# Kernel tuning notes

Measured on AMD Instinct MI355X. Metric: run time of the kernel, lower is better.

Reference implementation:

```python
import jax, jax.numpy as jnp
import numpy as np

N_NODES = 100000
N_EDGES = 1600000
NFEAT, NHID, NCLASS = 64, 128, 32


def _glorot(key, shape):
    fan_in, fan_out = shape[0], shape[1]
    lim = np.sqrt(6.0 / (fan_in + fan_out))
    return jax.random.uniform(key, shape, jnp.float32, -lim, lim)


def setup_inputs() -> dict:
    key = jax.random.key(0)
    ks = jax.random.split(key, 12)
    x = jax.random.normal(ks[0], (N_NODES, NFEAT), jnp.float32)
    edge_idx = jax.random.randint(ks[1], (2, N_EDGES), 0, N_NODES, jnp.int64)
    edge_weight = jax.random.uniform(ks[2], (N_EDGES,), jnp.float32)
    return {
        "x": x,
        "edge_idx": edge_idx,
        "edge_weight": edge_weight,
        # SAGEConv 1: out = mean_agg(x) @ Wl1 + b1 + x @ Wr1
        "Wl1": _glorot(ks[3], (NFEAT, NHID)),
        "Wr1": _glorot(ks[4], (NFEAT, NHID)),
        "b1": jnp.zeros((NHID,), jnp.float32),
        # SAGEConv 2
        "Wl2": _glorot(ks[5], (NHID, NHID)),
        "Wr2": _glorot(ks[6], (NHID, NHID)),
        "b2": jnp.zeros((NHID,), jnp.float32),
        # fc head: Linear(nhid, nclass) -> Linear(nclass, 1)
        "Wfc1": _glorot(ks[7], (NHID, NCLASS)),
        "bfc1": jnp.zeros((NCLASS,), jnp.float32),
        "Wfc2": _glorot(ks[8], (NCLASS, 1)),
        "bfc2": jnp.zeros((1,), jnp.float32),
    }


def _sage_conv(x, src, dst, Wl, Wr, b, n_nodes):
    # mean aggregation of source features at destination nodes
    msg_sum = jax.ops.segment_sum(x[src], dst, num_segments=n_nodes)  # [N, d]
    deg = jax.ops.segment_sum(jnp.ones((src.shape[0], 1), x.dtype), dst,
                              num_segments=n_nodes)                    # [N, 1]
    mean = msg_sum / jnp.maximum(deg, 1.0)
    return mean @ Wl + b + x @ Wr


def reference(x, edge_idx, edge_weight, Wl1, Wr1, b1, Wl2, Wr2, b2,
              Wfc1, bfc1, Wfc2, bfc2):
    n_nodes = x.shape[0]
    src, dst = edge_idx[0], edge_idx[1]
    # dropout is identity in eval mode (training=False)
    h = _sage_conv(x, src, dst, Wl1, Wr1, b1, n_nodes)   # [N, nhid]
    h = _sage_conv(h, src, dst, Wl2, Wr2, b2, n_nodes)   # [N, nhid]
    h = h @ Wfc1 + bfc1                                   # [N, nclass]
    out = h @ Wfc2 + bfc2                                 # [N, 1]
    return out
```

## Files before the change

kernel.cpp:

```cpp
#include <hip/hip_runtime.h>

#define S_NODES 512
#define S_SHIFT 9
#define CAP     10240
#define CHUNK   8192
#define NREP    4

__global__ __launch_bounds__(512) void fold_dots_kernel(
    const float* __restrict__ x,
    const float* __restrict__ Wl1, const float* __restrict__ Wr1, const float* __restrict__ b1,
    const float* __restrict__ Wl2, const float* __restrict__ Wr2, const float* __restrict__ b2,
    const float* __restrict__ Wfc1, const float* __restrict__ bfc1,
    const float* __restrict__ Wfc2, const float* __restrict__ bfc2,
    float* __restrict__ ga, float2* __restrict__ gbc, float* __restrict__ c01,
    int* __restrict__ cursor, int N)
{
    __shared__ float u[128], vl2[128], vr2[128], w2[32], wv[192];
    int t = threadIdx.x;
    if (blockIdx.x == 0 && t < 256) cursor[t] = 0;
    if (t < 32) w2[t] = Wfc2[t];
    __syncthreads();
    if (t < 128) {
        float s = 0.f;
        for (int k = 0; k < 32; ++k) s += Wfc1[t * 32 + k] * w2[k];
        u[t] = s;
    }
    __syncthreads();
    if (t < 128) {
        float a = 0.f, b = 0.f;
        for (int k = 0; k < 128; ++k) {
            a += Wl2[t * 128 + k] * u[k];
            b += Wr2[t * 128 + k] * u[k];
        }
        vl2[t] = a; vr2[t] = b;
    }
    __syncthreads();
    if (t < 64) {
        float wa = 0.f, wb = 0.f, wc = 0.f;
        for (int j = 0; j < 128; ++j) {
            float l1 = Wl1[t * 128 + j], r1 = Wr1[t * 128 + j];
            wc += l1 * vl2[j];
            wb += l1 * vr2[j] + r1 * vl2[j];
            wa += r1 * vr2[j];
        }
        wv[t] = wa; wv[64 + t] = wb; wv[128 + t] = wc;
    }
    if (blockIdx.x == 0 && t == 0) {
        float c0 = bfc2[0], c1 = 0.f;
        for (int j = 0; j < 128; ++j) {
            c0 += b1[j] * vr2[j] + b2[j] * u[j];
            c1 += b1[j] * vl2[j];
        }
        for (int k = 0; k < 32; ++k) c0 += bfc1[k] * w2[k];
        c01[0] = c0; c01[1] = c1;
    }
    __syncthreads();
    int lane = t & 63, sub = t >> 6;
    float wa = wv[lane], wb = wv[64 + lane], wc = wv[128 + lane];
    int ngroups = (N + 7) / 8;
    for (int g = blockIdx.x; g < ngroups; g += gridDim.x) {
        int node = g * 8 + sub;
        if (node >= N) continue;
        float v = x[(size_t)node * 64 + lane];
        float a = v * wa, b = v * wb, c = v * wc;
        for (int off = 32; off > 0; off >>= 1) {
            a += __shfl_down(a, off);
            b += __shfl_down(b, off);
            c += __shfl_down(c, off);
        }
        if (lane == 0) { ga[node] = a; gbc[node] = make_float2(b, c); }
    }
}

__global__ __launch_bounds__(256) void scatter_kernel(
    const int* __restrict__ src, const int* __restrict__ dst, int E, int B,
    int* __restrict__ cursor, unsigned* __restrict__ bucket)
{
    __shared__ int hist[256], lbase[256], lcur[256];
    int t = threadIdx.x;
    int e0 = blockIdx.x * CHUNK;
    int cnt = E - e0; if (cnt > CHUNK) cnt = CHUNK;
    hist[t] = 0;
    __syncthreads();
    for (int i = t; i < cnt; i += 256)
        atomicAdd(&hist[dst[e0 + i] >> S_SHIFT], 1);
    __syncthreads();
    if (t < B && hist[t] > 0) lbase[t] = atomicAdd(&cursor[t], hist[t]);
    lcur[t] = 0;
    __syncthreads();
    for (int i = t; i < cnt; i += 256) {
        int d = dst[e0 + i], s = src[e0 + i];
        int b = d >> S_SHIFT;
        int off = atomicAdd(&lcur[b], 1);
        bucket[(size_t)b * CAP + (unsigned)(lbase[b] + off)] =
            ((unsigned)s << S_SHIFT) | (unsigned)(d & (S_NODES - 1));
    }
}

__global__ __launch_bounds__(1024) void aggA_kernel(
    const unsigned* __restrict__ bucket, const int* __restrict__ cursor,
    const float2* __restrict__ gbc, const float* __restrict__ ga,
    const float* __restrict__ c01,
    float* __restrict__ q, float* __restrict__ t1, float* __restrict__ inv, int N)
{
    __shared__ float aB[NREP][S_NODES], aC[NREP][S_NODES];
    __shared__ int cnt[NREP][S_NODES];
    int t = threadIdx.x, b = blockIdx.x;
    int r = (t >> 6) & (NREP - 1);
    for (int i = t; i < NREP * S_NODES; i += 1024) {
        aB[0][i] = 0.f; aC[0][i] = 0.f; cnt[0][i] = 0;
    }
    __syncthreads();
    int n = cursor[b];
    const unsigned* bp = bucket + (size_t)b * CAP;
    for (int i = t; i < n; i += 1024) {
        unsigned uu = bp[i];
        float2 g = gbc[uu >> S_SHIFT];
        int dl = uu & (S_NODES - 1);
        atomicAdd(&aB[r][dl], g.x);
        atomicAdd(&aC[r][dl], g.y);
        atomicAdd(&cnt[r][dl], 1);
    }
    __syncthreads();
    if (t < S_NODES) {
        int node = (b << S_SHIFT) + t;
        if (node < N) {
            float sb = aB[0][t] + aB[1][t] + aB[2][t] + aB[3][t];
            float sc = aC[0][t] + aC[1][t] + aC[2][t] + aC[3][t];
            int d = cnt[0][t] + cnt[1][t] + cnt[2][t] + cnt[3][t];
            float iv = 1.0f / ((d > 0) ? (float)d : 1.0f);
            inv[node] = iv;
            q[node]   = iv * sc;
            t1[node]  = ga[node] + iv * sb + c01[0] + (d > 0 ? c01[1] : 0.f);
        }
    }
}

__global__ __launch_bounds__(1024) void aggB_kernel(
    const unsigned* __restrict__ bucket, const int* __restrict__ cursor,
    const float* __restrict__ q, const float* __restrict__ t1,
    const float* __restrict__ inv, float* __restrict__ out, int N)
{
    __shared__ float a2[NREP][S_NODES];
    int t = threadIdx.x, b = blockIdx.x;
    int r = (t >> 6) & (NREP - 1);
    for (int i = t; i < NREP * S_NODES; i += 1024) a2[0][i] = 0.f;
    __syncthreads();
    int n = cursor[b];
    const unsigned* bp = bucket + (size_t)b * CAP;
    for (int i = t; i < n; i += 1024) {
        unsigned uu = bp[i];
        atomicAdd(&a2[r][uu & (S_NODES - 1)], q[uu >> S_SHIFT]);
    }
    __syncthreads();
    if (t < S_NODES) {
        int node = (b << S_SHIFT) + t;
        if (node < N)
            out[node] = t1[node] + inv[node] * (a2[0][t] + a2[1][t] + a2[2][t] + a2[3][t]);
    }
}

extern "C" void kernel_launch(void* const* d_in, const int* in_sizes, int n_in,
                              void* d_out, int out_size, void* d_ws, size_t ws_size,
                              hipStream_t stream) {
    const float* x    = (const float*)d_in[0];
    const int*   eidx = (const int*)d_in[1];
    const float* Wl1  = (const float*)d_in[3];
    const float* Wr1  = (const float*)d_in[4];
    const float* b1   = (const float*)d_in[5];
    const float* Wl2  = (const float*)d_in[6];
    const float* Wr2  = (const float*)d_in[7];
    const float* b2   = (const float*)d_in[8];
    const float* Wfc1 = (const float*)d_in[9];
    const float* bfc1 = (const float*)d_in[10];
    const float* Wfc2 = (const float*)d_in[11];
    const float* bfc2 = (const float*)d_in[12];

    const int N = in_sizes[0] / 64;
    const int E = in_sizes[2];
    const int* src = eidx;
    const int* dst = eidx + E;
    const int B = (N + S_NODES - 1) / S_NODES;
    const int nscat = (E + CHUNK - 1) / CHUNK;

    char* ws = (char*)d_ws;
    int*      cursor = (int*)(ws);
    float*    c01    = (float*)(ws + 1024);
    float*    ga     = (float*)(ws + 2048);
    float*    q      = (float*)(ws + 2048 + (size_t)N * 4);
    float*    t1     = (float*)(ws + 2048 + (size_t)N * 8);
    float*    inv    = (float*)(ws + 2048 + (size_t)N * 12);
    float2*   gbc    = (float2*)(ws + 2048 + (size_t)N * 16);
    unsigned* bucket = (unsigned*)(ws + 2048 + (size_t)N * 24);

    fold_dots_kernel<<<256, 512, 0, stream>>>(
        x, Wl1, Wr1, b1, Wl2, Wr2, b2, Wfc1, bfc1, Wfc2, bfc2,
        ga, gbc, c01, cursor, N);

    scatter_kernel<<<nscat, 256, 0, stream>>>(src, dst, E, B, cursor, bucket);

    aggA_kernel<<<B, 1024, 0, stream>>>(bucket, cursor, gbc, ga, c01, q, t1, inv, N);
    aggB_kernel<<<B, 1024, 0, stream>>>(bucket, cursor, q, t1, inv, (float*)d_out, N);
}
```

Before: 201.2 us.

## Fuse all stages into one cooperative kernel with grid-wide syncs

Merges the weight folding, per-node dot products, edge bucketing and both aggregation passes into a single cooperative kernel separated by grid.sync, instead of four launches. t1 and inv now stay in shared memory between the two aggregation phases rather than going through global memory. The weight folding is rewritten with wave-level shuffle reductions, and the x dot products use float4 loads. The cursor reset moves to a hipMemsetAsync. In exchange, the grid is capped at 256 blocks of 1024 threads, so the scatter phase loses parallelism, and grid-wide barriers add their own cost.

```diff
diff --git a/kernel.cpp b/kernel.cpp
--- a/kernel.cpp
+++ b/kernel.cpp
@@ -1,162 +1,179 @@
 #include <hip/hip_runtime.h>
-
+#include <hip/hip_cooperative_groups.h>
+
+namespace cg = cooperative_groups;
+
+#define S_SHIFT 9
 #define S_NODES 512
-#define S_SHIFT 9
 #define CAP     10240
-#define CHUNK   8192
+#define CHUNK   2048
 #define NREP    4
-
-__global__ __launch_bounds__(512) void fold_dots_kernel(
+#define GRID    256
+#define BLK     1024
+
+__global__ __launch_bounds__(BLK, 4) void mega_kernel(
     const float* __restrict__ x,
+    const int* __restrict__ src, const int* __restrict__ dst,
+    int E, int N, int B, int nchunk,
+    int* __restrict__ cursor, unsigned* __restrict__ bucket,
     const float* __restrict__ Wl1, const float* __restrict__ Wr1, const float* __restrict__ b1,
     const float* __restrict__ Wl2, const float* __restrict__ Wr2, const float* __restrict__ b2,
     const float* __restrict__ Wfc1, const float* __restrict__ bfc1,
     const float* __restrict__ Wfc2, const float* __restrict__ bfc2,
-    float* __restrict__ ga, float2* __restrict__ gbc, float* __restrict__ c01,
-    int* __restrict__ cursor, int N)
+    float* __restrict__ ga, float2* __restrict__ gbc, float* __restrict__ q,
+    float* __restrict__ out)
 {
-    __shared__ float u[128], vl2[128], vr2[128], w2[32], wv[192];
+    __shared__ float wv[192], c01s[2];
+    __shared__ float uu[128], vl2[128], vr2[128], w2[32];
+    __shared__ int hist[256], lbase[256], lcur[256];
+    __shared__ float aB[NREP][S_NODES], aC[NREP][S_NODES];
+    __shared__ int cnts[NREP][S_NODES];
+    __shared__ float t1s[S_NODES], invs[S_NODES];
+
+    cg::grid_group grid = cg::this_grid();
     int t = threadIdx.x;
-    if (blockIdx.x == 0 && t < 256) cursor[t] = 0;
+    int l = t & 63;
+    int w = t >> 6;
+
     if (t < 32) w2[t] = Wfc2[t];
     __syncthreads();
-    if (t < 128) {
-        float s = 0.f;
-        for (int k = 0; k < 32; ++k) s += Wfc1[t * 32 + k] * w2[k];
-        u[t] = s;
-    }
-    __syncthreads();
-    if (t < 128) {
-        float a = 0.f, b = 0.f;
-        for (int k = 0; k < 128; ++k) {
-            a += Wl2[t * 128 + k] * u[k];
-            b += Wr2[t * 128 + k] * u[k];
-        }
-        vl2[t] = a; vr2[t] = b;
-    }
-    __syncthreads();
-    if (t < 64) {
-        float wa = 0.f, wb = 0.f, wc = 0.f;
-        for (int j = 0; j < 128; ++j) {
-            float l1 = Wl1[t * 128 + j], r1 = Wr1[t * 128 + j];
-            wc += l1 * vl2[j];
-            wb += l1 * vr2[j] + r1 * vl2[j];
-            wa += r1 * vr2[j];
-        }
-        wv[t] = wa; wv[64 + t] = wb; wv[128 + t] = wc;
-    }
-    if (blockIdx.x == 0 && t == 0) {
-        float c0 = bfc2[0], c1 = 0.f;
-        for (int j = 0; j < 128; ++j) {
-            c0 += b1[j] * vr2[j] + b2[j] * u[j];
-            c1 += b1[j] * vl2[j];
-        }
-        for (int k = 0; k < 32; ++k) c0 += bfc1[k] * w2[k];
-        c01[0] = c0; c01[1] = c1;
-    }
-    __syncthreads();
-    int lane = t & 63, sub = t >> 6;
-    float wa = wv[lane], wb = wv[64 + lane], wc = wv[128 + lane];
-    int ngroups = (N + 7) / 8;
-    for (int g = blockIdx.x; g < ngroups; g += gridDim.x) {
-        int node = g * 8 + sub;
-        if (node >= N) continue;
-        float v = x[(size_t)node * 64 + lane];
-        float a = v * wa, b = v * wb, c = v * wc;
-        for (int off = 32; off > 0; off >>= 1) {
-            a += __shfl_down(a, off);
-            b += __shfl_down(b, off);
-            c += __shfl_down(c, off);
-        }
-        if (lane == 0) { ga[node] = a; gbc[node] = make_float2(b, c); }
-    }
-}
-
-__global__ __launch_bounds__(256) void scatter_kernel(
-    const int* __restrict__ src, const int* __restrict__ dst, int E, int B,
-    int* __restrict__ cursor, unsigned* __restrict__ bucket)
-{
-    __shared__ int hist[256], lbase[256], lcur[256];
-    int t = threadIdx.x;
-    int e0 = blockIdx.x * CHUNK;
-    int cnt = E - e0; if (cnt > CHUNK) cnt = CHUNK;
-    hist[t] = 0;
-    __syncthreads();
-    for (int i = t; i < cnt; i += 256)
-        atomicAdd(&hist[dst[e0 + i] >> S_SHIFT], 1);
-    __syncthreads();
-    if (t < B && hist[t] > 0) lbase[t] = atomicAdd(&cursor[t], hist[t]);
-    lcur[t] = 0;
-    __syncthreads();
-    for (int i = t; i < cnt; i += 256) {
-        int d = dst[e0 + i], s = src[e0 + i];
-        int b = d >> S_SHIFT;
-        int off = atomicAdd(&lcur[b], 1);
-        bucket[(size_t)b * CAP + (unsigned)(lbase[b] + off)] =
-            ((unsigned)s << S_SHIFT) | (unsigned)(d & (S_NODES - 1));
-    }
-}
-
-__global__ __launch_bounds__(1024) void aggA_kernel(
-    const unsigned* __restrict__ bucket, const int* __restrict__ cursor,
-    const float2* __restrict__ gbc, const float* __restrict__ ga,
-    const float* __restrict__ c01,
-    float* __restrict__ q, float* __restrict__ t1, float* __restrict__ inv, int N)
-{
-    __shared__ float aB[NREP][S_NODES], aC[NREP][S_NODES];
-    __shared__ int cnt[NREP][S_NODES];
-    int t = threadIdx.x, b = blockIdx.x;
-    int r = (t >> 6) & (NREP - 1);
-    for (int i = t; i < NREP * S_NODES; i += 1024) {
-        aB[0][i] = 0.f; aC[0][i] = 0.f; cnt[0][i] = 0;
-    }
-    __syncthreads();
-    int n = cursor[b];
-    const unsigned* bp = bucket + (size_t)b * CAP;
-    for (int i = t; i < n; i += 1024) {
-        unsigned uu = bp[i];
-        float2 g = gbc[uu >> S_SHIFT];
-        int dl = uu & (S_NODES - 1);
-        atomicAdd(&aB[r][dl], g.x);
-        atomicAdd(&aC[r][dl], g.y);
-        atomicAdd(&cnt[r][dl], 1);
-    }
-    __syncthreads();
-    if (t < S_NODES) {
-        int node = (b << S_SHIFT) + t;
-        if (node < N) {
-            float sb = aB[0][t] + aB[1][t] + aB[2][t] + aB[3][t];
-            float sc = aC[0][t] + aC[1][t] + aC[2][t] + aC[3][t];
-            int d = cnt[0][t] + cnt[1][t] + cnt[2][t] + cnt[3][t];
-            float iv = 1.0f / ((d > 0) ? (float)d : 1.0f);
-            inv[node] = iv;
-            q[node]   = iv * sc;
-            t1[node]  = ga[node] + iv * sb + c01[0] + (d > 0 ? c01[1] : 0.f);
-        }
-    }
-}
-
-__global__ __launch_bounds__(1024) void aggB_kernel(
-    const unsigned* __restrict__ bucket, const int* __restrict__ cursor,
-    const float* __restrict__ q, const float* __restrict__ t1,
-    const float* __restrict__ inv, float* __restrict__ out, int N)
-{
-    __shared__ float a2[NREP][S_NODES];
-    int t = threadIdx.x, b = blockIdx.x;
-    int r = (t >> 6) & (NREP - 1);
-    for (int i = t; i < NREP * S_NODES; i += 1024) a2[0][i] = 0.f;
-    __syncthreads();
-    int n = cursor[b];
-    const unsigned* bp = bucket + (size_t)b * CAP;
-    for (int i = t; i < n; i += 1024) {
-        unsigned uu = bp[i];
-        atomicAdd(&a2[r][uu & (S_NODES - 1)], q[uu >> S_SHIFT]);
-    }
-    __syncthreads();
-    if (t < S_NODES) {
-        int node = (b << S_SHIFT) + t;
-        if (node < N)
-            out[node] = t1[node] + inv[node] * (a2[0][t] + a2[1][t] + a2[2][t] + a2[3][t]);
+    for (int j = 0; j < 8; ++j) {
+        int i = w + 16 * j;
+        float p = (l < 32) ? Wfc1[i * 32 + l] * w2[l] : 0.f;
+        for (int m = 16; m; m >>= 1) p += __shfl_xor(p, m);
+        if (l == 0) uu[i] = p;
+    }
+    __syncthreads();
+    for (int j = 0; j < 8; ++j) {
+        int i = w + 16 * j;
+        float ua = uu[l], ub = uu[64 + l];
+        float pa = Wl2[i * 128 + l] * ua + Wl2[i * 128 + 64 + l] * ub;
+        float pb = Wr2[i * 128 + l] * ua + Wr2[i * 128 + 64 + l] * ub;
+        for (int m = 32; m; m >>= 1) { pa += __shfl_xor(pa, m); pb += __shfl_xor(pb, m); }
+        if (l == 0) { vl2[i] = pa; vr2[i] = pb; }
+    }
+    __syncthreads();
+    for (int j = 0; j < 4; ++j) {
+        int i = w + 16 * j;
+        float l1a = Wl1[i * 128 + l],      l1b = Wl1[i * 128 + 64 + l];
+        float r1a = Wr1[i * 128 + l],      r1b = Wr1[i * 128 + 64 + l];
+        float La = vl2[l], Lb = vl2[64 + l], Ra = vr2[l], Rb = vr2[64 + l];
+        float pc = l1a * La + l1b * Lb;
+        float pb = l1a * Ra + l1b * Rb + r1a * La + r1b * Lb;
+        float pa = r1a * Ra + r1b * Rb;
+        for (int m = 32; m; m >>= 1) {
+            pa += __shfl_xor(pa, m); pb += __shfl_xor(pb, m); pc += __shfl_xor(pc, m);
+        }
+        if (l == 0) { wv[i] = pa; wv[64 + i] = pb; wv[128 + i] = pc; }
+    }
+    if (w == 15) {
+        float p0 = b1[l] * vr2[l] + b1[64 + l] * vr2[64 + l]
+                 + b2[l] * uu[l] + b2[64 + l] * uu[64 + l];
+        if (l < 32) p0 += bfc1[l] * w2[l];
+        float p1 = b1[l] * vl2[l] + b1[64 + l] * vl2[64 + l];
+        for (int m = 32; m; m >>= 1) { p0 += __shfl_xor(p0, m); p1 += __shfl_xor(p1, m); }
+        if (l == 0) { c01s[0] = p0 + bfc2[0]; c01s[1] = p1; }
+    }
+    __syncthreads();
+
+    {
+        int fp = l & 15, sub = l >> 4;
+        float4 wa4 = ((const float4*)wv)[fp];
+        float4 wb4 = ((const float4*)wv)[16 + fp];
+        float4 wc4 = ((const float4*)wv)[32 + fp];
+        const float4* x4 = (const float4*)x;
+        int Q = (N + 3) >> 2;
+        for (int qd = blockIdx.x * 16 + w; qd < Q; qd += GRID * 16) {
+            int node = qd * 4 + sub;
+            float a = 0.f, b = 0.f, c = 0.f;
+            if (node < N) {
+                float4 v = x4[(size_t)node * 16 + fp];
+                a = v.x * wa4.x + v.y * wa4.y + v.z * wa4.z + v.w * wa4.w;
+                b = v.x * wb4.x + v.y * wb4.y + v.z * wb4.z + v.w * wb4.w;
+                c = v.x * wc4.x + v.y * wc4.y + v.z * wc4.z + v.w * wc4.w;
+            }
+            for (int m = 8; m; m >>= 1) {
+                a += __shfl_xor(a, m); b += __shfl_xor(b, m); c += __shfl_xor(c, m);
+            }
+            if (fp == 0 && node < N) { ga[node] = a; gbc[node] = make_float2(b, c); }
+        }
+    }
+
+    for (int ch = blockIdx.x; ch < nchunk; ch += GRID) {
+        int e0 = ch * CHUNK;
+        int cnt = E - e0; if (cnt > CHUNK) cnt = CHUNK;
+        if (t < 256) hist[t] = 0;
+        __syncthreads();
+        for (int i = t; i < cnt; i += BLK)
+            atomicAdd(&hist[dst[e0 + i] >> S_SHIFT], 1);
+        __syncthreads();
+        if (t < 256) {
+            lcur[t] = 0;
+            if (t < B && hist[t] > 0) lbase[t] = atomicAdd(&cursor[t], hist[t]);
+        }
+        __syncthreads();
+        for (int i = t; i < cnt; i += BLK) {
+            int d = dst[e0 + i], s = src[e0 + i];
+            int bb = d >> S_SHIFT;
+            int off = atomicAdd(&lcur[bb], 1);
+            bucket[(size_t)bb * CAP + (unsigned)(lbase[bb] + off)] =
+                ((unsigned)s << S_SHIFT) | (unsigned)(d & (S_NODES - 1));
+        }
+        __syncthreads();
+    }
+
+    grid.sync();
+
+    int b = blockIdx.x;
+    int r = w & (NREP - 1);
+    if (b < B) {
+        float* aBf = (float*)aB; float* aCf = (float*)aC; int* cnf = (int*)cnts;
+        for (int i = t; i < NREP * S_NODES; i += BLK) { aBf[i] = 0.f; aCf[i] = 0.f; cnf[i] = 0; }
+        __syncthreads();
+        int n = cursor[b];
+        const unsigned* bp = bucket + (size_t)b * CAP;
+        for (int i = t; i < n; i += BLK) {
+            unsigned pe = bp[i];
+            float2 g = gbc[pe >> S_SHIFT];
+            int dl = pe & (S_NODES - 1);
+            atomicAdd(&aB[r][dl], g.x);
+            atomicAdd(&aC[r][dl], g.y);
+            atomicAdd(&cnts[r][dl], 1);
+        }
+        __syncthreads();
+        if (t < S_NODES) {
+            int node = (b << S_SHIFT) + t;
+            if (node < N) {
+                float sb = aB[0][t] + aB[1][t] + aB[2][t] + aB[3][t];
+                float sc = aC[0][t] + aC[1][t] + aC[2][t] + aC[3][t];
+                int d = cnts[0][t] + cnts[1][t] + cnts[2][t] + cnts[3][t];
+                float iv = 1.0f / ((d > 0) ? (float)d : 1.0f);
+                invs[t] = iv;
+                q[node] = iv * sc;
+                t1s[t] = ga[node] + iv * sb + c01s[0] + (d > 0 ? c01s[1] : 0.f);
+            }
+        }
+    }
+
+    grid.sync();
+
+    if (b < B) {
+        float* a2 = (float*)aB;
+        for (int i = t; i < NREP * S_NODES; i += BLK) a2[i] = 0.f;
+        __syncthreads();
+        int n = cursor[b];
+        const unsigned* bp = bucket + (size_t)b * CAP;
+        for (int i = t; i < n; i += BLK) {
+            unsigned pe = bp[i];
+            atomicAdd(&a2[r * S_NODES + (pe & (S_NODES - 1))], q[pe >> S_SHIFT]);
+        }
+        __syncthreads();
+        if (t < S_NODES) {
+            int node = (b << S_SHIFT) + t;
+            if (node < N)
+                out[node] = t1s[t] + invs[t] *
+                    (a2[t] + a2[S_NODES + t] + a2[2 * S_NODES + t] + a2[3 * S_NODES + t]);
+        }
     }
 }
 
@@ -176,29 +193,26 @@
     const float* Wfc2 = (const float*)d_in[11];
     const float* bfc2 = (const float*)d_in[12];
 
-    const int N = in_sizes[0] / 64;
-    const int E = in_sizes[2];
+    int N = in_sizes[0] / 64;
+    int E = in_sizes[2];
     const int* src = eidx;
     const int* dst = eidx + E;
-    const int B = (N + S_NODES - 1) / S_NODES;
-    const int nscat = (E + CHUNK - 1) / CHUNK;
+    int B = (N + S_NODES - 1) / S_NODES;
+    int nchunk = (E + CHUNK - 1) / CHUNK;
 
     char* ws = (char*)d_ws;
     int*      cursor = (int*)(ws);
-    float*    c01    = (float*)(ws + 1024);
-    float*    ga     = (float*)(ws + 2048);
-    float*    q      = (float*)(ws + 2048 + (size_t)N * 4);
-    float*    t1     = (float*)(ws + 2048 + (size_t)N * 8);
-    float*    inv    = (float*)(ws + 2048 + (size_t)N * 12);
-    float2*   gbc    = (float2*)(ws + 2048 + (size_t)N * 16);
-    unsigned* bucket = (unsigned*)(ws + 2048 + (size_t)N * 24);
-
-    fold_dots_kernel<<<256, 512, 0, stream>>>(
-        x, Wl1, Wr1, b1, Wl2, Wr2, b2, Wfc1, bfc1, Wfc2, bfc2,
-        ga, gbc, c01, cursor, N);
-
-    scatter_kernel<<<nscat, 256, 0, stream>>>(src, dst, E, B, cursor, bucket);
-
-    aggA_kernel<<<B, 1024, 0, stream>>>(bucket, cursor, gbc, ga, c01, q, t1, inv, N);
-    aggB_kernel<<<B, 1024, 0, stream>>>(bucket, cursor, q, t1, inv, (float*)d_out, N);
+    float*    ga     = (float*)(ws + 1024);
+    float*    q      = (float*)(ws + 1024 + (size_t)N * 4);
+    float2*   gbc    = (float2*)(ws + 1024 + (size_t)N * 8);
+    unsigned* bucket = (unsigned*)(ws + 1024 + (size_t)N * 16);
+    float*    out    = (float*)d_out;
+
+    hipMemsetAsync(cursor, 0, 1024, stream);
+
+    void* args[] = { &x, &src, &dst, &E, &N, &B, &nchunk, &cursor, &bucket,
+                     &Wl1, &Wr1, &b1, &Wl2, &Wr2, &b2, &Wfc1, &bfc1, &Wfc2, &bfc2,
+                     &ga, &gbc, &q, &out };
+    hipLaunchCooperativeKernel((void*)mega_kernel, dim3(GRID), dim3(BLK),
+                               args, 0, stream);
 }
```

Result: slower. 273.1 us (+35.8%).

## Parallelize weight folding across wavefronts and vectorize per-node dot products

Applied to the files above, without the earlier changes.

The serial per-thread matrix-vector folds in the prologue are replaced with wavefront-parallel dot products that use xor-shuffle reductions, so the redundant per-block weight preprocessing finishes sooner. The per-node projection of x now loads float4s and handles four nodes per wavefront with 16-lane reductions instead of one node per wavefront with 64-lane reductions. The fold kernel moves to 1024 threads per block and the scatter chunk size is halved, giving more scatter blocks. The shared-memory zeroing loops are rewritten with flat pointers, which does not change behavior.

```diff
diff --git a/kernel.cpp b/kernel.cpp
--- a/kernel.cpp
+++ b/kernel.cpp
@@ -1,12 +1,13 @@
 #include <hip/hip_runtime.h>
 
+#define S_SHIFT 9
 #define S_NODES 512
-#define S_SHIFT 9
 #define CAP     10240
-#define CHUNK   8192
+#define CHUNK   4096
 #define NREP    4
-
-__global__ __launch_bounds__(512) void fold_dots_kernel(
+#define DGRID   256
+
+__global__ __launch_bounds__(1024) void fold_dots_kernel(
     const float* __restrict__ x,
     const float* __restrict__ Wl1, const float* __restrict__ Wr1, const float* __restrict__ b1,
     const float* __restrict__ Wl2, const float* __restrict__ Wr2, const float* __restrict__ b2,
@@ -15,60 +16,73 @@
     float* __restrict__ ga, float2* __restrict__ gbc, float* __restrict__ c01,
     int* __restrict__ cursor, int N)
 {
-    __shared__ float u[128], vl2[128], vr2[128], w2[32], wv[192];
+    __shared__ float wv[192];
+    __shared__ float uu[128], vl2[128], vr2[128], w2[32];
     int t = threadIdx.x;
+    int l = t & 63;
+    int w = t >> 6;
+
     if (blockIdx.x == 0 && t < 256) cursor[t] = 0;
     if (t < 32) w2[t] = Wfc2[t];
     __syncthreads();
-    if (t < 128) {
-        float s = 0.f;
-        for (int k = 0; k < 32; ++k) s += Wfc1[t * 32 + k] * w2[k];
-        u[t] = s;
-    }
-    __syncthreads();
-    if (t < 128) {
-        float a = 0.f, b = 0.f;
-        for (int k = 0; k < 128; ++k) {
-            a += Wl2[t * 128 + k] * u[k];
-            b += Wr2[t * 128 + k] * u[k];
-        }
-        vl2[t] = a; vr2[t] = b;
-    }
-    __syncthreads();
-    if (t < 64) {
-        float wa = 0.f, wb = 0.f, wc = 0.f;
-        for (int j = 0; j < 128; ++j) {
-            float l1 = Wl1[t * 128 + j], r1 = Wr1[t * 128 + j];
-            wc += l1 * vl2[j];
-            wb += l1 * vr2[j] + r1 * vl2[j];
-            wa += r1 * vr2[j];
-        }
-        wv[t] = wa; wv[64 + t] = wb; wv[128 + t] = wc;
-    }
-    if (blockIdx.x == 0 && t == 0) {
-        float c0 = bfc2[0], c1 = 0.f;
-        for (int j = 0; j < 128; ++j) {
-            c0 += b1[j] * vr2[j] + b2[j] * u[j];
-            c1 += b1[j] * vl2[j];
-        }
-        for (int k = 0; k < 32; ++k) c0 += bfc1[k] * w2[k];
-        c01[0] = c0; c01[1] = c1;
-    }
-    __syncthreads();
-    int lane = t & 63, sub = t >> 6;
-    float wa = wv[lane], wb = wv[64 + lane], wc = wv[128 + lane];
-    int ngroups = (N + 7) / 8;
-    for (int g = blockIdx.x; g < ngroups; g += gridDim.x) {
-        int node = g * 8 + sub;
-        if (node >= N) continue;
-        float v = x[(size_t)node * 64 + lane];
-        float a = v * wa, b = v * wb, c = v * wc;
-        for (int off = 32; off > 0; off >>= 1) {
-            a += __shfl_down(a, off);
-            b += __shfl_down(b, off);
-            c += __shfl_down(c, off);
-        }
-        if (lane == 0) { ga[node] = a; gbc[node] = make_float2(b, c); }
+    for (int j = 0; j < 8; ++j) {
+        int i = w + 16 * j;
+        float p = (l < 32) ? Wfc1[i * 32 + l] * w2[l] : 0.f;
+        for (int m = 16; m; m >>= 1) p += __shfl_xor(p, m);
+        if (l == 0) uu[i] = p;
+    }
+    __syncthreads();
+    for (int j = 0; j < 8; ++j) {
+        int i = w + 16 * j;
+        float ua = uu[l], ub = uu[64 + l];
+        float pa = Wl2[i * 128 + l] * ua + Wl2[i * 128 + 64 + l] * ub;
+        float pb = Wr2[i * 128 + l] * ua + Wr2[i * 128 + 64 + l] * ub;
+        for (int m = 32; m; m >>= 1) { pa += __shfl_xor(pa, m); pb += __shfl_xor(pb, m); }
+        if (l == 0) { vl2[i] = pa; vr2[i] = pb; }
+    }
+    __syncthreads();
+    for (int j = 0; j < 4; ++j) {
+        int i = w + 16 * j;
+        float l1a = Wl1[i * 128 + l], l1b = Wl1[i * 128 + 64 + l];
+        float r1a = Wr1[i * 128 + l], r1b = Wr1[i * 128 + 64 + l];
+        float La = vl2[l], Lb = vl2[64 + l], Ra = vr2[l], Rb = vr2[64 + l];
+        float pc = l1a * La + l1b * Lb;
+        float pb = l1a * Ra + l1b * Rb + r1a * La + r1b * Lb;
+        float pa = r1a * Ra + r1b * Rb;
+        for (int m = 32; m; m >>= 1) {
+            pa += __shfl_xor(pa, m); pb += __shfl_xor(pb, m); pc += __shfl_xor(pc, m);
+        }
+        if (l == 0) { wv[i] = pa; wv[64 + i] = pb; wv[128 + i] = pc; }
+    }
+    if (blockIdx.x == 0 && w == 15) {
+        float p0 = b1[l] * vr2[l] + b1[64 + l] * vr2[64 + l]
+                 + b2[l] * uu[l] + b2[64 + l] * uu[64 + l];
+        if (l < 32) p0 += bfc1[l] * w2[l];
+        float p1 = b1[l] * vl2[l] + b1[64 + l] * vl2[64 + l];
+        for (int m = 32; m; m >>= 1) { p0 += __shfl_xor(p0, m); p1 += __shfl_xor(p1, m); }
+        if (l == 0) { c01[0] = p0 + bfc2[0]; c01[1] = p1; }
+    }
+    __syncthreads();
+
+    int fp = l & 15, sub = l >> 4;
+    float4 wa4 = ((const float4*)wv)[fp];
+    float4 wb4 = ((const float4*)wv)[16 + fp];
+    float4 wc4 = ((const float4*)wv)[32 + fp];
+    const float4* x4 = (const float4*)x;
+    int Q = (N + 3) >> 2;
+    for (int qd = blockIdx.x * 16 + w; qd < Q; qd += DGRID * 16) {
+        int node = qd * 4 + sub;
+        float a = 0.f, b = 0.f, c = 0.f;
+        if (node < N) {
+            float4 v = x4[(size_t)node * 16 + fp];
+            a = v.x * wa4.x + v.y * wa4.y + v.z * wa4.z + v.w * wa4.w;
+            b = v.x * wb4.x + v.y * wb4.y + v.z * wb4.z + v.w * wb4.w;
+            c = v.x * wc4.x + v.y * wc4.y + v.z * wc4.z + v.w * wc4.w;
+        }
+        for (int m = 8; m; m >>= 1) {
+            a += __shfl_xor(a, m); b += __shfl_xor(b, m); c += __shfl_xor(c, m);
+        }
+        if (fp == 0 && node < N) { ga[node] = a; gbc[node] = make_float2(b, c); }
     }
 }
 
@@ -107,9 +121,8 @@
     __shared__ int cnt[NREP][S_NODES];
     int t = threadIdx.x, b = blockIdx.x;
     int r = (t >> 6) & (NREP - 1);
-    for (int i = t; i < NREP * S_NODES; i += 1024) {
-        aB[0][i] = 0.f; aC[0][i] = 0.f; cnt[0][i] = 0;
-    }
+    float* aBf = (float*)aB; float* aCf = (float*)aC; int* cnf = (int*)cnt;
+    for (int i = t; i < NREP * S_NODES; i += 1024) { aBf[i] = 0.f; aCf[i] = 0.f; cnf[i] = 0; }
     __syncthreads();
     int n = cursor[b];
     const unsigned* bp = bucket + (size_t)b * CAP;
@@ -144,7 +157,8 @@
     __shared__ float a2[NREP][S_NODES];
     int t = threadIdx.x, b = blockIdx.x;
     int r = (t >> 6) & (NREP - 1);
-    for (int i = t; i < NREP * S_NODES; i += 1024) a2[0][i] = 0.f;
+    float* a2f = (float*)a2;
+    for (int i = t; i < NREP * S_NODES; i += 1024) a2f[i] = 0.f;
     __syncthreads();
     int n = cursor[b];
     const unsigned* bp = bucket + (size_t)b * CAP;
@@ -193,7 +207,7 @@
     float2*   gbc    = (float2*)(ws + 2048 + (size_t)N * 16);
     unsigned* bucket = (unsigned*)(ws + 2048 + (size_t)N * 24);
 
-    fold_dots_kernel<<<256, 512, 0, stream>>>(
+    fold_dots_kernel<<<DGRID, 1024, 0, stream>>>(
         x, Wl1, Wr1, b1, Wl2, Wr2, b2, Wfc1, bfc1, Wfc2, bfc2,
         ga, gbc, c01, cursor, N);
 
```

Measured after the change: 174.5 us. 1.15x faster.
